# Performance work log

Measured on AMD Instinct MI355X. Metric: run time of the kernel, lower is better.

Reference implementation:

```python
import jax, jax.numpy as jnp
import numpy as np

HEADS = 4
DIM_HEAD = 128


def setup_inputs() -> dict:
    key = jax.random.key(0)
    k1, k2, k3, k4 = jax.random.split(key, 4)
    B, C, H, W = 8, 256, 64, 64
    hidden = HEADS * DIM_HEAD  # 512
    x = jax.random.normal(k1, (B, C, H, W), dtype=jnp.float32)
    # 1x1 convs are just channel matmuls; store kernels as [out_ch, in_ch]
    w_qkv = jax.random.normal(k2, (3 * hidden, C), dtype=jnp.float32) * 0.05
    w_out = jax.random.normal(k3, (C, hidden), dtype=jnp.float32) * 0.05
    b_out = jax.random.normal(k4, (C,), dtype=jnp.float32) * 0.05
    return {"x": x, "w_qkv": w_qkv, "w_out": w_out, "b_out": b_out}


def reference(x, w_qkv, w_out, b_out):
    B, C, H, W = x.shape
    n = H * W
    # to_qkv: 1x1 conv without bias == channel matmul
    qkv = jnp.einsum('bchw,oc->bohw', x, w_qkv)  # [B, 3*heads*dim_head, H, W]
    qkv = qkv.reshape(B, 3, HEADS, DIM_HEAD, n)  # 'b (qkv heads c) h w -> b qkv heads c n'
    q, k, v = qkv[:, 0], qkv[:, 1], qkv[:, 2]    # each [B, heads, dim_head, n]
    k = jax.nn.softmax(k, axis=-1)               # softmax over spatial positions
    context = jnp.einsum('bhdn,bhen->bhde', k, v)   # [B, heads, d, e]
    out = jnp.einsum('bhde,bhdn->bhen', context, q)  # [B, heads, e, n]
    out = out.reshape(B, HEADS * DIM_HEAD, H, W)
    # to_out: 1x1 conv with bias
    return jnp.einsum('bchw,oc->bohw', out, w_out) + b_out[None, :, None, None]
```

## Files before the change

### kernel.cpp

```cpp
#include <hip/hip_runtime.h>
#include <stdint.h>


using frag8 = __attribute__((ext_vector_type(8))) short;
using f32x4 = __attribute__((ext_vector_type(4))) float;

__device__ __forceinline__ unsigned short f2bf(float f) {
    union { float f; unsigned int u; } c; c.f = f;
    unsigned int u = c.u;
    return (unsigned short)((u + 0x7FFFu + ((u >> 16) & 1u)) >> 16);
}

__device__ __forceinline__ void gl_lds16(const void* g, void* l) {
    __builtin_amdgcn_global_load_lds(
        (const __attribute__((address_space(1))) unsigned int*)g,
        (__attribute__((address_space(3))) unsigned int*)l, 16, 0, 0);
}

__global__ __launch_bounds__(256) void k0_prep(
    const float* __restrict__ x, const float* __restrict__ w_qkv,
    const float* __restrict__ w_out,
    unsigned short* __restrict__ xbT, unsigned short* __restrict__ wkvb,
    unsigned short* __restrict__ woutb, unsigned short* __restrict__ wqT)
{
    __shared__ float T[64][65];
    const int tid = threadIdx.x;
    const int blk0 = blockIdx.x;
    if (blk0 < 2048) {
        const int n0 = (blk0 & 63) * 64, c0 = ((blk0 >> 6) & 3) * 64, b = blk0 >> 8;
        const float* xb = x + (size_t)b * 1048576;
        const int cr = tid >> 4, nc = (tid & 15) * 4;
        #pragma unroll
        for (int p = 0; p < 4; ++p) {
            float4 v = *(const float4*)(xb + (size_t)(c0 + cr + p * 16) * 4096 + n0 + nc);
            T[cr + p * 16][nc + 0] = v.x; T[cr + p * 16][nc + 1] = v.y;
            T[cr + p * 16][nc + 2] = v.z; T[cr + p * 16][nc + 3] = v.w;
        }
        __syncthreads();
        const int n = tid >> 2, cc = (tid & 3) * 16;
        unsigned short* dst = xbT + (size_t)b * 1048576 + (size_t)(n0 + n) * 256 + c0 + cc;
        #pragma unroll
        for (int g = 0; g < 4; ++g) {
            ushort4 o;
            o.x = f2bf(T[cc + g * 4 + 0][n]);
            o.y = f2bf(T[cc + g * 4 + 1][n]);
            o.z = f2bf(T[cc + g * 4 + 2][n]);
            o.w = f2bf(T[cc + g * 4 + 3][n]);
            *(ushort4*)(dst + g * 4) = o;
        }
        return;
    }
    const int blk = blk0 - 2048;
    if (blk < 256) {
        const int idx = (blk * 256 + tid) * 4;
        float4 v = *(const float4*)(w_qkv + 512 * 256 + idx);
        ushort4 o;
        o.x = f2bf(v.x); o.y = f2bf(v.y); o.z = f2bf(v.z); o.w = f2bf(v.w);
        *(ushort4*)(wkvb + idx) = o;
    } else if (blk < 384) {
        const int idx = ((blk - 256) * 256 + tid) * 4;
        float4 v = *(const float4*)(w_out + idx);
        ushort4 o;
        o.x = f2bf(v.x); o.y = f2bf(v.y); o.z = f2bf(v.z); o.w = f2bf(v.w);
        *(ushort4*)(woutb + idx) = o;
    } else {
        const int t = blk - 384;
        const int j0 = (t >> 2) * 64, c0 = (t & 3) * 64;
        const int r = tid >> 4, cc = (tid & 15) * 4;
        #pragma unroll
        for (int p = 0; p < 4; ++p) {
            float4 v = *(const float4*)(w_qkv + (j0 + r + p * 16) * 256 + c0 + cc);
            T[r + p * 16][cc + 0] = v.x; T[r + p * 16][cc + 1] = v.y;
            T[r + p * 16][cc + 2] = v.z; T[r + p * 16][cc + 3] = v.w;
        }
        __syncthreads();
        const int c = tid >> 2, jj = (tid & 3) * 16;
        #pragma unroll
        for (int g = 0; g < 4; ++g) {
            ushort4 o;
            o.x = f2bf(T[jj + g * 4 + 0][c]);
            o.y = f2bf(T[jj + g * 4 + 1][c]);
            o.z = f2bf(T[jj + g * 4 + 2][c]);
            o.w = f2bf(T[jj + g * 4 + 3][c]);
            *(ushort4*)(wqT + (c0 + c) * 512 + j0 + jj + g * 4) = o;
        }
    }
}

__global__ __launch_bounds__(256) void k1p(
    const unsigned short* __restrict__ wkvb,
    const unsigned short* __restrict__ xbT,
    unsigned short* __restrict__ kv, float* __restrict__ rowsum)
{
    __shared__ unsigned short Wl[32768];
    __shared__ unsigned short Xs[2][4096];
    const int tid  = threadIdx.x;
    const int w = tid >> 6, lane = tid & 63;
    const int quad = lane >> 4, l16 = lane & 15;
    const int wm = (w >> 1) * 64, wn = (w & 1) * 64;
    const int ns = blockIdx.x, rb = blockIdx.y, b = blockIdx.z;

    const unsigned short* Wg = wkvb + (size_t)(rb * 128) * 256;
    const unsigned short* Xb = xbT + (size_t)b * 1048576 + (size_t)ns * 131072;

    const int c0 = w * 128 + lane, c1 = c0 + 64;
    const int r0 = c0 >> 2, s0 = ((c0 & 3) ^ ((r0 >> 1) & 3)) * 8;
    const int r1 = c1 >> 2, s1 = ((c1 & 3) ^ ((r1 >> 1) & 3)) * 8;
    const int ldsw = w * 1024;

    #pragma unroll
    for (int ks = 0; ks < 8; ++ks) {
        gl_lds16(Wg + (size_t)r0 * 256 + ks * 32 + s0, &Wl[ks * 4096 + ldsw]);
        gl_lds16(Wg + (size_t)r1 * 256 + ks * 32 + s1, &Wl[ks * 4096 + ldsw + 512]);
    }
    const unsigned short* gX0 = Xb + (size_t)r0 * 256 + s0;
    const unsigned short* gX1 = Xb + (size_t)r1 * 256 + s1;
#define STGX(T) do { \
        const int o_ = ((T) >> 3) * 32768 + ((T) & 7) * 32; \
        gl_lds16(gX0 + o_, &Xs[(T) & 1][ldsw]); \
        gl_lds16(gX1 + o_, &Xs[(T) & 1][ldsw + 512]); } while (0)
    STGX(0); STGX(1);
    asm volatile("s_waitcnt vmcnt(0)" ::: "memory");
    __builtin_amdgcn_sched_barrier(0);
    __builtin_amdgcn_s_barrier();
    __builtin_amdgcn_sched_barrier(0);

    float rsum[4][4] = {};
    f32x4 acc[4][4] = {};
    unsigned short* Cb = kv + (size_t)b * 4194304 + (size_t)(rb * 128) * 4096 + ns * 512;

    #pragma unroll 2
    for (int t = 0; t < 32; ++t) {
        const unsigned short* xs = Xs[t & 1];
        const unsigned short* wl = &Wl[(t & 7) * 4096];
        frag8 a[4], bb[4];
        #pragma unroll
        for (int tt = 0; tt < 4; ++tt) {
            const int rn = wn + tt * 16 + l16;
            bb[tt] = *(const frag8*)(xs + rn * 32 + ((quad ^ ((rn >> 1) & 3)) << 3));
        }
        #pragma unroll
        for (int tt = 0; tt < 4; ++tt) {
            const int ra = wm + tt * 16 + l16;
            a[tt] = *(const frag8*)(wl + ra * 32 + ((quad ^ ((ra >> 1) & 3)) << 3));
        }
        asm volatile("s_waitcnt lgkmcnt(0)" ::: "memory");
        __builtin_amdgcn_sched_barrier(0);
        __builtin_amdgcn_s_barrier();
        __builtin_amdgcn_sched_barrier(0);
        if (t + 2 < 32) STGX(t + 2);
        #pragma unroll
        for (int mt = 0; mt < 4; ++mt)
            #pragma unroll
            for (int nt = 0; nt < 4; ++nt)
                acc[mt][nt] = __builtin_amdgcn_mfma_f32_16x16x32_bf16(
                    a[mt], bb[nt], acc[mt][nt], 0, 0, 0);
        if ((t & 7) == 7) {
            unsigned short* C = Cb + (t >> 3) * 128;
            if (rb < 4) {
                #pragma unroll
                for (int mt = 0; mt < 4; ++mt) {
                    const int row = wm + mt * 16 + quad * 4;
                    #pragma unroll
                    for (int nt = 0; nt < 4; ++nt) {
                        const int col = wn + nt * 16 + l16;
                        #pragma unroll
                        for (int r = 0; r < 4; ++r) {
                            float e = __expf(acc[mt][nt][r]);
                            rsum[mt][r] += e;
                            C[(size_t)(row + r) * 4096 + col] = f2bf(e);
                        }
                    }
                }
            } else {
                #pragma unroll
                for (int mt = 0; mt < 4; ++mt) {
                    const int row = wm + mt * 16 + quad * 4;
                    #pragma unroll
                    for (int nt = 0; nt < 4; ++nt) {
                        const int col = wn + nt * 16 + l16;
                        #pragma unroll
                        for (int r = 0; r < 4; ++r)
                            C[(size_t)(row + r) * 4096 + col] = f2bf(acc[mt][nt][r]);
                    }
                }
            }
            #pragma unroll
            for (int mt = 0; mt < 4; ++mt)
                #pragma unroll
                for (int nt = 0; nt < 4; ++nt)
                    acc[mt][nt] = (f32x4){0.f, 0.f, 0.f, 0.f};
            asm volatile("s_waitcnt vmcnt(0)" ::: "memory");
        } else if (t + 2 < 32) {
            asm volatile("s_waitcnt vmcnt(2)" ::: "memory");
        } else {
            asm volatile("s_waitcnt vmcnt(0)" ::: "memory");
        }
        __builtin_amdgcn_sched_barrier(0);
        __builtin_amdgcn_s_barrier();
        __builtin_amdgcn_sched_barrier(0);
    }
#undef STGX
    if (rb < 4) {
        float* rs = rowsum + b * 512 + rb * 128;
        #pragma unroll
        for (int mt = 0; mt < 4; ++mt) {
            const int row = wm + mt * 16 + quad * 4;
            #pragma unroll
            for (int r = 0; r < 4; ++r) {
                float v = rsum[mt][r];
                v += __shfl_xor(v, 1, 64);
                v += __shfl_xor(v, 2, 64);
                v += __shfl_xor(v, 4, 64);
                v += __shfl_xor(v, 8, 64);
                if (l16 == 0) atomicAdd(rs + row + r, v);
            }
        }
    }
}

template<int MODE>
__global__ __launch_bounds__(256) void mfma_bt(
    const unsigned short* __restrict__ A0, int lda,
    const unsigned short* __restrict__ B0, int ldb,
    void* __restrict__ C0, int ldc,
    const float* __restrict__ bias, int Kp,
    unsigned long long sAz, unsigned long long sBz, unsigned long long sCz)
{
    __shared__ unsigned short As[2][4096];
    __shared__ unsigned short Bs[2][4096];
    const int tid  = threadIdx.x;
    const int w    = tid >> 6, lane = tid & 63;
    const int quad = lane >> 4, l16 = lane & 15;
    const int wm = (w >> 1) * 64, wn = (w & 1) * 64;
    const int z = blockIdx.z;

    const unsigned short* A;
    const unsigned short* B;
    int m0, n0, ks, NS;
    if constexpr (MODE == 2) {
        m0 = 0; n0 = 0;
        ks = blockIdx.x * 512; NS = 16;
        const unsigned long long off =
            ((unsigned long long)(z >> 2) * 1024ull + (unsigned long long)(z & 3) * 128ull) * 4096ull;
        A = A0 + off; B = B0 + off;
    } else if constexpr (MODE == 3) {
        m0 = blockIdx.y * 128; n0 = 0;
        ks = 0; NS = Kp >> 5;
        A = A0 + (unsigned long long)(z & 3) * 128ull + (unsigned long long)m0 * lda;
        B = B0 + (unsigned long long)z * 16384ull;
    } else {
        m0 = blockIdx.y * 128; n0 = blockIdx.x * 128;
        ks = 0; NS = Kp >> 5;
        A = A0 + sAz * z + (unsigned long long)m0 * lda;
        B = B0 + sBz * z + (unsigned long long)n0 * ldb;
    }

    const int c0 = w * 128 + lane, c1 = c0 + 64;
    const int r0 = c0 >> 2, s0 = ((c0 & 3) ^ ((r0 >> 1) & 3)) * 8;
    const int r1 = c1 >> 2, s1 = ((c1 & 3) ^ ((r1 >> 1) & 3)) * 8;
    const unsigned short* gA0 = A + (unsigned long long)r0 * lda + s0 + ks;
    const unsigned short* gA1 = A + (unsigned long long)r1 * lda + s1 + ks;
    const unsigned short* gB0 = B + (unsigned long long)r0 * ldb + s0 + ks;
    const unsigned short* gB1 = B + (unsigned long long)r1 * ldb + s1 + ks;
    const int ldsw = w * 1024;

#define STG(T) do { \
        const int kk_ = (T) * 32; \
        gl_lds16(gA0 + kk_, &As[(T) & 1][ldsw]); \
        gl_lds16(gA1 + kk_, &As[(T) & 1][ldsw + 512]); \
        gl_lds16(gB0 + kk_, &Bs[(T) & 1][ldsw]); \
        gl_lds16(gB1 + kk_, &Bs[(T) & 1][ldsw + 512]); } while (0)

    STG(0); STG(1);
    asm volatile("s_waitcnt vmcnt(0)" ::: "memory");
    __builtin_amdgcn_sched_barrier(0);
    __builtin_amdgcn_s_barrier();
    __builtin_amdgcn_sched_barrier(0);

    f32x4 acc[4][4] = {};

    for (int t = 0; t < NS; ++t) {
        const unsigned short* as = As[t & 1];
        const unsigned short* bs = Bs[t & 1];
        frag8 a[4], bb[4];
        #pragma unroll
        for (int tt = 0; tt < 4; ++tt) {
            const int ra = wm + tt * 16 + l16;
            const int rn = wn + tt * 16 + l16;
            a[tt]  = *(const frag8*)(as + ra * 32 + ((quad ^ ((ra >> 1) & 3)) << 3));
            bb[tt] = *(const frag8*)(bs + rn * 32 + ((quad ^ ((rn >> 1) & 3)) << 3));
        }
        asm volatile("s_waitcnt lgkmcnt(0)" ::: "memory");
        __builtin_amdgcn_sched_barrier(0);
        __builtin_amdgcn_s_barrier();
        __builtin_amdgcn_sched_barrier(0);
        if (t + 2 < NS) STG(t + 2);
        #pragma unroll
        for (int mt = 0; mt < 4; ++mt)
            #pragma unroll
            for (int nt = 0; nt < 4; ++nt)
                acc[mt][nt] = __builtin_amdgcn_mfma_f32_16x16x32_bf16(
                    a[mt], bb[nt], acc[mt][nt], 0, 0, 0);
        if (t + 2 < NS) {
            asm volatile("s_waitcnt vmcnt(4)" ::: "memory");
        } else {
            asm volatile("s_waitcnt vmcnt(0)" ::: "memory");
        }
        __builtin_amdgcn_sched_barrier(0);
        __builtin_amdgcn_s_barrier();
        __builtin_amdgcn_sched_barrier(0);
    }
#undef STG

    if constexpr (MODE == 0 || MODE == 3) {
        unsigned short* C;
        if constexpr (MODE == 0)
            C = (unsigned short*)C0 + sCz * z + (unsigned long long)m0 * ldc + n0;
        else
            C = (unsigned short*)C0 + (unsigned long long)(z >> 2) * 131072ull
              + (unsigned long long)(z & 3) * 128ull + (unsigned long long)m0 * ldc;
        #pragma unroll
        for (int mt = 0; mt < 4; ++mt) {
            const int row = wm + mt * 16 + quad * 4;
            #pragma unroll
            for (int nt = 0; nt < 4; ++nt) {
                const int col = wn + nt * 16 + l16;
                #pragma unroll
                for (int r = 0; r < 4; ++r)
                    C[(unsigned long long)(row + r) * ldc + col] = f2bf(acc[mt][nt][r]);
            }
        }
    } else if constexpr (MODE == 1) {
        float* C = (float*)C0 + sCz * z + (unsigned long long)m0 * ldc + n0;
        const float* bp = bias + m0;
        #pragma unroll
        for (int mt = 0; mt < 4; ++mt) {
            const int row = wm + mt * 16 + quad * 4;
            #pragma unroll
            for (int nt = 0; nt < 4; ++nt) {
                const int col = wn + nt * 16 + l16;
                #pragma unroll
                for (int r = 0; r < 4; ++r)
                    C[(unsigned long long)(row + r) * ldc + col] = acc[mt][nt][r] + bp[row + r];
            }
        }
    } else {
        float* C = (float*)C0 + (unsigned long long)z * 16384ull;
        #pragma unroll
        for (int mt = 0; mt < 4; ++mt) {
            const int row = wm + mt * 16 + quad * 4;
            #pragma unroll
            for (int nt = 0; nt < 4; ++nt) {
                const int col = wn + nt * 16 + l16;
                #pragma unroll
                for (int r = 0; r < 4; ++r)
                    atomicAdd(C + (row + r) * 128 + col, acc[mt][nt][r]);
            }
        }
    }
}

__global__ __launch_bounds__(256) void k3_scale(
    const float* __restrict__ ctx, const float* __restrict__ rowsum,
    unsigned short* __restrict__ ctxb)
{
    const int idx = (blockIdx.x * 256 + threadIdx.x) * 4;
    const float inv = 1.0f / rowsum[idx >> 7];
    float4 t = *(const float4*)(ctx + idx);
    ushort4 o;
    o.x = f2bf(t.x * inv); o.y = f2bf(t.y * inv);
    o.z = f2bf(t.z * inv); o.w = f2bf(t.w * inv);
    *(ushort4*)(ctxb + idx) = o;
}

extern "C" void kernel_launch(void* const* d_in, const int* in_sizes, int n_in,
                              void* d_out, int out_size, void* d_ws, size_t ws_size,
                              hipStream_t stream) {
    (void)in_sizes; (void)n_in; (void)out_size; (void)ws_size;
    const float* x     = (const float*)d_in[0];
    const float* w_qkv = (const float*)d_in[1];
    const float* w_out = (const float*)d_in[2];
    const float* b_out = (const float*)d_in[3];
    float* out = (float*)d_out;

    char* ws = (char*)d_ws;
    unsigned short* xbT    = (unsigned short*)ws;
    unsigned short* wkvb   = (unsigned short*)(ws + 16777216);
    unsigned short* woutb  = (unsigned short*)(ws + 17301504);
    unsigned short* wqT    = (unsigned short*)(ws + 17563648);
    float*          ctx    = (float*)(ws + 17825792);
    float*          rowsum = (float*)(ws + 19922944);
    unsigned short* ctxb   = (unsigned short*)(ws + 19939328);
    unsigned short* Mb     = (unsigned short*)(ws + 20987904);
    unsigned short* Nb     = (unsigned short*)(ws + 23085056);
    unsigned short* kv     = (unsigned short*)(ws + 24133632);

    hipMemsetAsync(ws + 17825792, 0, 2097152 + 16384, stream);

    k0_prep<<<dim3(2464), 256, 0, stream>>>(x, w_qkv, w_out, xbT, wkvb, woutb, wqT);
    k1p<<<dim3(8, 8, 8), 256, 0, stream>>>(wkvb, xbT, kv, rowsum);
    mfma_bt<2><<<dim3(8, 1, 32), 256, 0, stream>>>(
        kv, 4096, kv + (size_t)512 * 4096, 4096, ctx, 128, nullptr, 0,
        0ull, 0ull, 0ull);
    k3_scale<<<dim3(512), 256, 0, stream>>>(ctx, rowsum, ctxb);
    mfma_bt<3><<<dim3(1, 2, 32), 256, 0, stream>>>(
        woutb, 512, ctxb, 128, Mb, 512, nullptr, 128,
        0ull, 0ull, 0ull);
    mfma_bt<0><<<dim3(2, 2, 8), 256, 0, stream>>>(
        Mb, 512, wqT, 512, Nb, 256, nullptr, 512,
        131072ull, 0ull, 65536ull);
    mfma_bt<1><<<dim3(32, 2, 8), 256, 0, stream>>>(
        Nb, 256, xbT, 256, out, 4096, b_out, 256,
        65536ull, 1048576ull, 1048576ull);
}
```

Measured before the change: 198.1 us.

## Read X fragments directly from global in KV GEMM and add split-K context kernel

The KV projection kernel no longer stages X tiles through double-buffered LDS with barriers. Instead each wave loads its B fragments straight from global memory, looping over four column sub-blocks. The context GEMM (MODE 2) is replaced by a new kernel, k3r, with finer split-K (16 slices of 256) that loads both operands directly from global with no LDS and accumulates into the output with atomics. This removes LDS staging and synchronization overhead but depends on cache behaviour for operand reuse, and the loads are no longer coalesced or overlapped with compute.

```diff
diff --git a/kernel.cpp b/kernel.cpp
--- a/kernel.cpp
+++ b/kernel.cpp
@@ -87,13 +87,12 @@
     }
 }
 
-__global__ __launch_bounds__(256) void k1p(
+__global__ __launch_bounds__(256) void k1r(
     const unsigned short* __restrict__ wkvb,
     const unsigned short* __restrict__ xbT,
     unsigned short* __restrict__ kv, float* __restrict__ rowsum)
 {
     __shared__ unsigned short Wl[32768];
-    __shared__ unsigned short Xs[2][4096];
     const int tid  = threadIdx.x;
     const int w = tid >> 6, lane = tid & 63;
     const int quad = lane >> 4, l16 = lane & 15;
@@ -107,100 +106,78 @@
     const int r0 = c0 >> 2, s0 = ((c0 & 3) ^ ((r0 >> 1) & 3)) * 8;
     const int r1 = c1 >> 2, s1 = ((c1 & 3) ^ ((r1 >> 1) & 3)) * 8;
     const int ldsw = w * 1024;
-
     #pragma unroll
     for (int ks = 0; ks < 8; ++ks) {
         gl_lds16(Wg + (size_t)r0 * 256 + ks * 32 + s0, &Wl[ks * 4096 + ldsw]);
         gl_lds16(Wg + (size_t)r1 * 256 + ks * 32 + s1, &Wl[ks * 4096 + ldsw + 512]);
     }
-    const unsigned short* gX0 = Xb + (size_t)r0 * 256 + s0;
-    const unsigned short* gX1 = Xb + (size_t)r1 * 256 + s1;
-#define STGX(T) do { \
-        const int o_ = ((T) >> 3) * 32768 + ((T) & 7) * 32; \
-        gl_lds16(gX0 + o_, &Xs[(T) & 1][ldsw]); \
-        gl_lds16(gX1 + o_, &Xs[(T) & 1][ldsw + 512]); } while (0)
-    STGX(0); STGX(1);
     asm volatile("s_waitcnt vmcnt(0)" ::: "memory");
     __builtin_amdgcn_sched_barrier(0);
     __builtin_amdgcn_s_barrier();
-    __builtin_amdgcn_sched_barrier(0);
 
     float rsum[4][4] = {};
-    f32x4 acc[4][4] = {};
-    unsigned short* Cb = kv + (size_t)b * 4194304 + (size_t)(rb * 128) * 4096 + ns * 512;
-
-    #pragma unroll 2
-    for (int t = 0; t < 32; ++t) {
-        const unsigned short* xs = Xs[t & 1];
-        const unsigned short* wl = &Wl[(t & 7) * 4096];
-        frag8 a[4], bb[4];
-        #pragma unroll
-        for (int tt = 0; tt < 4; ++tt) {
-            const int rn = wn + tt * 16 + l16;
-            bb[tt] = *(const frag8*)(xs + rn * 32 + ((quad ^ ((rn >> 1) & 3)) << 3));
-        }
-        #pragma unroll
-        for (int tt = 0; tt < 4; ++tt) {
-            const int ra = wm + tt * 16 + l16;
-            a[tt] = *(const frag8*)(wl + ra * 32 + ((quad ^ ((ra >> 1) & 3)) << 3));
-        }
-        asm volatile("s_waitcnt lgkmcnt(0)" ::: "memory");
-        __builtin_amdgcn_sched_barrier(0);
-        __builtin_amdgcn_s_barrier();
-        __builtin_amdgcn_sched_barrier(0);
-        if (t + 2 < 32) STGX(t + 2);
-        #pragma unroll
-        for (int mt = 0; mt < 4; ++mt)
+    unsigned short* Cb = kv + (size_t)b * 4194304 + (size_t)(rb * 128) * 4096
+                       + (size_t)ns * 512;
+
+    #pragma unroll 1
+    for (int nsub = 0; nsub < 4; ++nsub) {
+        const unsigned short* px[4];
+        #pragma unroll
+        for (int nt = 0; nt < 4; ++nt)
+            px[nt] = Xb + (size_t)(nsub * 128 + wn + nt * 16 + l16) * 256 + quad * 8;
+
+        f32x4 acc[4][4] = {};
+        #pragma unroll
+        for (int ks = 0; ks < 8; ++ks) {
+            frag8 a[4], bb[4];
             #pragma unroll
             for (int nt = 0; nt < 4; ++nt)
-                acc[mt][nt] = __builtin_amdgcn_mfma_f32_16x16x32_bf16(
-                    a[mt], bb[nt], acc[mt][nt], 0, 0, 0);
-        if ((t & 7) == 7) {
-            unsigned short* C = Cb + (t >> 3) * 128;
-            if (rb < 4) {
-                #pragma unroll
-                for (int mt = 0; mt < 4; ++mt) {
-                    const int row = wm + mt * 16 + quad * 4;
-                    #pragma unroll
-                    for (int nt = 0; nt < 4; ++nt) {
-                        const int col = wn + nt * 16 + l16;
-                        #pragma unroll
-                        for (int r = 0; r < 4; ++r) {
-                            float e = __expf(acc[mt][nt][r]);
-                            rsum[mt][r] += e;
-                            C[(size_t)(row + r) * 4096 + col] = f2bf(e);
-                        }
-                    }
-                }
-            } else {
-                #pragma unroll
-                for (int mt = 0; mt < 4; ++mt) {
-                    const int row = wm + mt * 16 + quad * 4;
-                    #pragma unroll
-                    for (int nt = 0; nt < 4; ++nt) {
-                        const int col = wn + nt * 16 + l16;
-                        #pragma unroll
-                        for (int r = 0; r < 4; ++r)
-                            C[(size_t)(row + r) * 4096 + col] = f2bf(acc[mt][nt][r]);
-                    }
-                }
+                bb[nt] = *(const frag8*)(px[nt] + ks * 32);
+            #pragma unroll
+            for (int mt = 0; mt < 4; ++mt) {
+                const int ra = wm + mt * 16 + l16;
+                a[mt] = *(const frag8*)(Wl + ks * 4096 + ra * 32
+                                        + ((quad ^ ((ra >> 1) & 3)) << 3));
             }
             #pragma unroll
             for (int mt = 0; mt < 4; ++mt)
                 #pragma unroll
                 for (int nt = 0; nt < 4; ++nt)
-                    acc[mt][nt] = (f32x4){0.f, 0.f, 0.f, 0.f};
-            asm volatile("s_waitcnt vmcnt(0)" ::: "memory");
-        } else if (t + 2 < 32) {
-            asm volatile("s_waitcnt vmcnt(2)" ::: "memory");
+                    acc[mt][nt] = __builtin_amdgcn_mfma_f32_16x16x32_bf16(
+                        a[mt], bb[nt], acc[mt][nt], 0, 0, 0);
+        }
+
+        unsigned short* C = Cb + nsub * 128;
+        if (rb < 4) {
+            #pragma unroll
+            for (int mt = 0; mt < 4; ++mt) {
+                const int row = wm + mt * 16 + quad * 4;
+                #pragma unroll
+                for (int nt = 0; nt < 4; ++nt) {
+                    const int col = wn + nt * 16 + l16;
+                    #pragma unroll
+                    for (int r = 0; r < 4; ++r) {
+                        float e = __expf(acc[mt][nt][r]);
+                        rsum[mt][r] += e;
+                        C[(size_t)(row + r) * 4096 + col] = f2bf(e);
+                    }
+                }
+            }
         } else {
-            asm volatile("s_waitcnt vmcnt(0)" ::: "memory");
-        }
-        __builtin_amdgcn_sched_barrier(0);
-        __builtin_amdgcn_s_barrier();
-        __builtin_amdgcn_sched_barrier(0);
-    }
-#undef STGX
+            #pragma unroll
+            for (int mt = 0; mt < 4; ++mt) {
+                const int row = wm + mt * 16 + quad * 4;
+                #pragma unroll
+                for (int nt = 0; nt < 4; ++nt) {
+                    const int col = wn + nt * 16 + l16;
+                    #pragma unroll
+                    for (int r = 0; r < 4; ++r)
+                        C[(size_t)(row + r) * 4096 + col] = f2bf(acc[mt][nt][r]);
+                }
+            }
+        }
+    }
+
     if (rb < 4) {
         float* rs = rowsum + b * 512 + rb * 128;
         #pragma unroll
@@ -215,6 +192,58 @@
                 v += __shfl_xor(v, 8, 64);
                 if (l16 == 0) atomicAdd(rs + row + r, v);
             }
+        }
+    }
+}
+
+__global__ __launch_bounds__(256) void k3r(
+    const unsigned short* __restrict__ kv, float* __restrict__ ctx)
+{
+    const int tid  = threadIdx.x;
+    const int w = tid >> 6, lane = tid & 63;
+    const int quad = lane >> 4, l16 = lane & 15;
+    const int wm = (w >> 1) * 64, wn = (w & 1) * 64;
+    const int sl = blockIdx.x, z = blockIdx.y;
+
+    const size_t off = (size_t)(z >> 2) * 4194304ull + (size_t)(z & 3) * 524288ull;
+    const unsigned short* Ab = kv + off;
+    const unsigned short* Bb = kv + off + 2097152ull;
+    const int k0 = sl * 256;
+
+    const unsigned short* pa[4];
+    const unsigned short* pb[4];
+    #pragma unroll
+    for (int t = 0; t < 4; ++t) {
+        pa[t] = Ab + (size_t)(wm + t * 16 + l16) * 4096 + k0 + quad * 8;
+        pb[t] = Bb + (size_t)(wn + t * 16 + l16) * 4096 + k0 + quad * 8;
+    }
+
+    f32x4 acc[4][4] = {};
+    #pragma unroll
+    for (int ks = 0; ks < 8; ++ks) {
+        frag8 a[4], bb[4];
+        #pragma unroll
+        for (int t = 0; t < 4; ++t) a[t]  = *(const frag8*)(pa[t] + ks * 32);
+        #pragma unroll
+        for (int t = 0; t < 4; ++t) bb[t] = *(const frag8*)(pb[t] + ks * 32);
+        #pragma unroll
+        for (int mt = 0; mt < 4; ++mt)
+            #pragma unroll
+            for (int nt = 0; nt < 4; ++nt)
+                acc[mt][nt] = __builtin_amdgcn_mfma_f32_16x16x32_bf16(
+                    a[mt], bb[nt], acc[mt][nt], 0, 0, 0);
+    }
+
+    float* C = ctx + (size_t)z * 16384ull;
+    #pragma unroll
+    for (int mt = 0; mt < 4; ++mt) {
+        const int row = wm + mt * 16 + quad * 4;
+        #pragma unroll
+        for (int nt = 0; nt < 4; ++nt) {
+            const int col = wn + nt * 16 + l16;
+            #pragma unroll
+            for (int r = 0; r < 4; ++r)
+                atomicAdd(C + (row + r) * 128 + col, acc[mt][nt][r]);
         }
     }
 }
@@ -237,21 +266,15 @@
 
     const unsigned short* A;
     const unsigned short* B;
-    int m0, n0, ks, NS;
-    if constexpr (MODE == 2) {
-        m0 = 0; n0 = 0;
-        ks = blockIdx.x * 512; NS = 16;
-        const unsigned long long off =
-            ((unsigned long long)(z >> 2) * 1024ull + (unsigned long long)(z & 3) * 128ull) * 4096ull;
-        A = A0 + off; B = B0 + off;
-    } else if constexpr (MODE == 3) {
+    int m0, n0, NS;
+    if constexpr (MODE == 3) {
         m0 = blockIdx.y * 128; n0 = 0;
-        ks = 0; NS = Kp >> 5;
+        NS = Kp >> 5;
         A = A0 + (unsigned long long)(z & 3) * 128ull + (unsigned long long)m0 * lda;
         B = B0 + (unsigned long long)z * 16384ull;
     } else {
         m0 = blockIdx.y * 128; n0 = blockIdx.x * 128;
-        ks = 0; NS = Kp >> 5;
+        NS = Kp >> 5;
         A = A0 + sAz * z + (unsigned long long)m0 * lda;
         B = B0 + sBz * z + (unsigned long long)n0 * ldb;
     }
@@ -259,10 +282,10 @@
     const int c0 = w * 128 + lane, c1 = c0 + 64;
     const int r0 = c0 >> 2, s0 = ((c0 & 3) ^ ((r0 >> 1) & 3)) * 8;
     const int r1 = c1 >> 2, s1 = ((c1 & 3) ^ ((r1 >> 1) & 3)) * 8;
-    const unsigned short* gA0 = A + (unsigned long long)r0 * lda + s0 + ks;
-    const unsigned short* gA1 = A + (unsigned long long)r1 * lda + s1 + ks;
-    const unsigned short* gB0 = B + (unsigned long long)r0 * ldb + s0 + ks;
-    const unsigned short* gB1 = B + (unsigned long long)r1 * ldb + s1 + ks;
+    const unsigned short* gA0 = A + (unsigned long long)r0 * lda + s0;
+    const unsigned short* gA1 = A + (unsigned long long)r1 * lda + s1;
+    const unsigned short* gB0 = B + (unsigned long long)r0 * ldb + s0;
+    const unsigned short* gB1 = B + (unsigned long long)r1 * ldb + s1;
     const int ldsw = w * 1024;
 
 #define STG(T) do { \
@@ -331,7 +354,7 @@
                     C[(unsigned long long)(row + r) * ldc + col] = f2bf(acc[mt][nt][r]);
             }
         }
-    } else if constexpr (MODE == 1) {
+    } else {
         float* C = (float*)C0 + sCz * z + (unsigned long long)m0 * ldc + n0;
         const float* bp = bias + m0;
         #pragma unroll
@@ -343,19 +366,6 @@
                 #pragma unroll
                 for (int r = 0; r < 4; ++r)
                     C[(unsigned long long)(row + r) * ldc + col] = acc[mt][nt][r] + bp[row + r];
-            }
-        }
-    } else {
-        float* C = (float*)C0 + (unsigned long long)z * 16384ull;
-        #pragma unroll
-        for (int mt = 0; mt < 4; ++mt) {
-            const int row = wm + mt * 16 + quad * 4;
-            #pragma unroll
-            for (int nt = 0; nt < 4; ++nt) {
-                const int col = wn + nt * 16 + l16;
-                #pragma unroll
-                for (int r = 0; r < 4; ++r)
-                    atomicAdd(C + (row + r) * 128 + col, acc[mt][nt][r]);
             }
         }
     }
@@ -399,10 +409,8 @@
     hipMemsetAsync(ws + 17825792, 0, 2097152 + 16384, stream);
 
     k0_prep<<<dim3(2464), 256, 0, stream>>>(x, w_qkv, w_out, xbT, wkvb, woutb, wqT);
-    k1p<<<dim3(8, 8, 8), 256, 0, stream>>>(wkvb, xbT, kv, rowsum);
-    mfma_bt<2><<<dim3(8, 1, 32), 256, 0, stream>>>(
-        kv, 4096, kv + (size_t)512 * 4096, 4096, ctx, 128, nullptr, 0,
-        0ull, 0ull, 0ull);
+    k1r<<<dim3(8, 8, 8), 256, 0, stream>>>(wkvb, xbT, kv, rowsum);
+    k3r<<<dim3(16, 32), 256, 0, stream>>>(kv, ctx);
     k3_scale<<<dim3(512), 256, 0, stream>>>(ctx, rowsum, ctxb);
     mfma_bt<3><<<dim3(1, 2, 32), 256, 0, stream>>>(
         woutb, 512, ctxb, 128, Mb, 512, nullptr, 128,
```

After: 214.3 us. 8.2% more time.
